# Optimization experiments

Measured on AMD Instinct MI355X. Metric: run time of the kernel, lower is better.

Reference implementation:

```python
import jax, jax.numpy as jnp
import numpy as np

B, T, D = 2, 2048, 1024
H, G, K = 16, 4, 64          # num_heads, num_kv_heads, head_dim
R = H // G                   # GQA repeat factor
F = 4096                     # mlp_dim
EPS = 1e-6


def rms_norm(x, scale, eps=EPS):
    var = jnp.mean(x.astype(jnp.float32) ** 2, axis=-1, keepdims=True)
    normed = x * jax.lax.rsqrt(var + eps)
    return (scale * normed).astype(x.dtype)


def apply_rope(x_BTHK, sin_BTK, cos_BTK):
    half = x_BTHK.shape[-1] // 2
    x1, x2 = x_BTHK[..., :half], x_BTHK[..., half:]
    s = sin_BTK[:, :, None, :]
    c = cos_BTK[:, :, None, :]
    return jnp.concatenate([x1 * c - x2 * s, x2 * c + x1 * s], axis=-1).astype(x_BTHK.dtype)


def setup_inputs() -> dict:
    key = jax.random.key(0)
    ks = jax.random.split(key, 12)
    hidden_BTD = jax.random.normal(ks[0], (B, T, D), jnp.float32)
    # rope tables: realistic sin/cos of position*inv_freq
    inv_freq = 1.0 / (10000.0 ** (jnp.arange(K // 2, dtype=jnp.float32) / (K // 2)))
    ang = jnp.arange(T, dtype=jnp.float32)[:, None] * inv_freq[None, :]  # [T, K/2]
    sin_BTK = jnp.broadcast_to(jnp.sin(ang)[None], (B, T, K // 2))
    cos_BTK = jnp.broadcast_to(jnp.cos(ang)[None], (B, T, K // 2))
    mask = jnp.broadcast_to(jnp.tril(jnp.ones((T, T), bool))[None], (B, T, T))
    sc = 1.0 / np.sqrt(D)
    scf = 1.0 / np.sqrt(F)
    return {
        "hidden_BTD": hidden_BTD, "sin_BTK": sin_BTK, "cos_BTK": cos_BTK, "mask": mask,
        "ln1_scale": jnp.ones((D,), jnp.float32),
        "ln2_scale": jnp.ones((D,), jnp.float32),
        "qn_scale": jnp.ones((K,), jnp.float32),
        "kn_scale": jnp.ones((K,), jnp.float32),
        "q_w": jax.random.normal(ks[1], (D, H * K), jnp.float32) * sc,
        "k_w": jax.random.normal(ks[2], (D, G * K), jnp.float32) * sc,
        "v_w": jax.random.normal(ks[3], (D, G * K), jnp.float32) * sc,
        "o_w": jax.random.normal(ks[4], (H * K, D), jnp.float32) * sc,
        "gate_w": jax.random.normal(ks[5], (D, F), jnp.float32) * sc,
        "up_w": jax.random.normal(ks[6], (D, F), jnp.float32) * sc,
        "down_w": jax.random.normal(ks[7], (F, D), jnp.float32) * scf,
    }


def reference(hidden_BTD, sin_BTK, cos_BTK, mask, ln1_scale, ln2_scale,
              qn_scale, kn_scale, q_w, k_w, v_w, o_w, gate_w, up_w, down_w):
    x = rms_norm(hidden_BTD, ln1_scale)
    q = rms_norm((x @ q_w).reshape(B, T, H, K), qn_scale)
    k = rms_norm((x @ k_w).reshape(B, T, G, K), kn_scale)
    v = (x @ v_w).reshape(B, T, G, K)
    q = apply_rope(q, sin_BTK, cos_BTK)
    k = apply_rope(k, sin_BTK, cos_BTK)
    q_BTGRK = q.reshape(B, T, G, R, K)
    scale = K ** (-0.5)
    logits = jnp.einsum('BTGRK,BSGK->BTSGR', q_BTGRK, k) * scale
    neg = float(jnp.finfo(logits.dtype).min)
    logits = jnp.where(mask[:, :, :, None, None], logits, neg)
    weights = jax.nn.softmax(logits.astype(jnp.float32), axis=2).astype(logits.dtype)
    attn = jnp.einsum('BTSGR,BSGK->BTGRK', weights, v).reshape(B, T, H * K)
    hidden_BTD = hidden_BTD + attn @ o_w
    y = rms_norm(hidden_BTD, ln2_scale)
    ff = (jax.nn.silu(y @ gate_w) * (y @ up_w)) @ down_w
    return hidden_BTD + ff
```

## Files before the change

kernel.cpp:

```cpp
#include <hip/hip_runtime.h>
#include <hip/hip_bf16.h>

#define EPSF 1e-6f
constexpr int Bsz  = 2;
constexpr int Tseq = 2048;
constexpr int Dmod = 1024;
constexpr int Hh   = 16;
constexpr int Gg   = 4;
constexpr int Ff   = 4096;
constexpr int Mrows = Bsz * Tseq;
constexpr int QKVN = 1536;

typedef __attribute__((ext_vector_type(8))) short bf16x8;
typedef __attribute__((ext_vector_type(4))) float f32x4;
typedef unsigned short u16;

__device__ inline u16 f2bf(float x) {
    union { float f; unsigned u; } v; v.f = x;
    unsigned r = v.u + 0x7fff + ((v.u >> 16) & 1);
    return (u16)(r >> 16);
}
__device__ inline float bf2f(u16 h) {
    union { unsigned u; float f; } v; v.u = ((unsigned)h) << 16; return v.f;
}

__device__ __forceinline__ void async_copy16(const u16* g, u16* l) {
    __builtin_amdgcn_global_load_lds(
        (const __attribute__((address_space(1))) void*)g,
        (__attribute__((address_space(3))) void*)l, 16, 0, 0);
}


template <int LO>
__global__ __launch_bounds__(256) void wprep_kernel(
    const float* __restrict__ W, u16* __restrict__ Th, u16* __restrict__ Tl,
    int Kd, int N)
{
    __shared__ float tile[32][33];
    const int n0 = blockIdx.x * 32, k0 = blockIdx.y * 32;
    const int r = threadIdx.x >> 3, c4 = (threadIdx.x & 7) * 4;
    const float4 v = *reinterpret_cast<const float4*>(&W[(size_t)(k0 + r) * N + n0 + c4]);
    tile[r][c4 + 0] = v.x; tile[r][c4 + 1] = v.y;
    tile[r][c4 + 2] = v.z; tile[r][c4 + 3] = v.w;
    __syncthreads();
    const int nl = threadIdx.x >> 3, kq = (threadIdx.x & 7) * 4;
    float x0 = tile[kq + 0][nl], x1 = tile[kq + 1][nl];
    float x2 = tile[kq + 2][nl], x3 = tile[kq + 3][nl];
    ushort4 h;
    h.x = f2bf(x0); h.y = f2bf(x1); h.z = f2bf(x2); h.w = f2bf(x3);
    *reinterpret_cast<ushort4*>(&Th[(size_t)(n0 + nl) * Kd + k0 + kq]) = h;
    if (LO) {
        ushort4 l;
        l.x = f2bf(x0 - bf2f(h.x)); l.y = f2bf(x1 - bf2f(h.y));
        l.z = f2bf(x2 - bf2f(h.z)); l.w = f2bf(x3 - bf2f(h.w));
        *reinterpret_cast<ushort4*>(&Tl[(size_t)(n0 + nl) * Kd + k0 + kq]) = l;
    }
}

template <int LO>
__global__ __launch_bounds__(256) void rmsnorm_split_kernel(
    const float* __restrict__ x, const float* __restrict__ scale,
    u16* __restrict__ oh, u16* __restrict__ ol)
{
    const int row = blockIdx.x;
    const int tid = threadIdx.x;
    const float4 v = reinterpret_cast<const float4*>(x + (size_t)row * Dmod)[tid];
    float ss = v.x * v.x + v.y * v.y + v.z * v.z + v.w * v.w;
    #pragma unroll
    for (int off = 32; off; off >>= 1) ss += __shfl_xor(ss, off, 64);
    __shared__ float part[4];
    if ((tid & 63) == 0) part[tid >> 6] = ss;
    __syncthreads();
    const float tot = part[0] + part[1] + part[2] + part[3];
    const float rstd = rsqrtf(tot * (1.0f / Dmod) + EPSF);
    const float4 sc = reinterpret_cast<const float4*>(scale)[tid];
    float o0 = v.x * rstd * sc.x, o1 = v.y * rstd * sc.y;
    float o2 = v.z * rstd * sc.z, o3 = v.w * rstd * sc.w;
    ushort4 h;
    h.x = f2bf(o0); h.y = f2bf(o1); h.z = f2bf(o2); h.w = f2bf(o3);
    *reinterpret_cast<ushort4*>(&oh[(size_t)row * Dmod + tid * 4]) = h;
    if (LO) {
        ushort4 l;
        l.x = f2bf(o0 - bf2f(h.x)); l.y = f2bf(o1 - bf2f(h.y));
        l.z = f2bf(o2 - bf2f(h.z)); l.w = f2bf(o3 - bf2f(h.w));
        *reinterpret_cast<ushort4*>(&ol[(size_t)row * Dmod + tid * 4]) = l;
    }
}

template <int ASPLIT, int BSPLIT, int RES>
__global__ __launch_bounds__(256, 2) void mfma_gemm_kernel(
    const u16* __restrict__ Ah, const u16* __restrict__ Al,
    const u16* __restrict__ Bh, const u16* __restrict__ Bl,
    const float* __restrict__ res, float* __restrict__ C,
    int M, int N, int Kd)
{
    __shared__ u16 As_h[128 * 32];
    __shared__ u16 As_l[128 * 32];
    __shared__ u16 Bs_h[128 * 32];
    __shared__ u16 Bs_l[128 * 32];

    const int tid = threadIdx.x;
    const int lane = tid & 63, wave = tid >> 6;
    const int wm = (wave >> 1) * 64, wn = (wave & 1) * 64;
    const int m0 = blockIdx.y * 128, n0 = blockIdx.x * 128;
    const int fm = lane & 15, quad = lane >> 4;
    const int fsw = (fm >> 1) & 3;
    const int fcol = ((quad ^ fsw) * 8);

    f32x4 acc[4][4];
    #pragma unroll
    for (int i = 0; i < 4; ++i)
        #pragma unroll
        for (int j = 0; j < 4; ++j) acc[i][j] = (f32x4){0.f, 0.f, 0.f, 0.f};

    const int lrow = lane >> 2;
    const int lchunk = lane & 3;
    const int schunk = lchunk ^ ((lrow >> 1) & 3);

    for (int k0 = 0; k0 < Kd; k0 += 32) {
        __syncthreads();
        #pragma unroll
        for (int p = 0; p < 2; ++p) {
            const int row = wave * 32 + p * 16 + lrow;
            const size_t ga = (size_t)(m0 + row) * Kd + k0 + schunk * 8;
            const size_t gb = (size_t)(n0 + row) * Kd + k0 + schunk * 8;
            const int ls = row * 32 + lchunk * 8;
            async_copy16(&Ah[ga], &As_h[ls]);
            if (ASPLIT) async_copy16(&Al[ga], &As_l[ls]);
            async_copy16(&Bh[gb], &Bs_h[ls]);
            if (BSPLIT) async_copy16(&Bl[gb], &Bs_l[ls]);
        }
        __syncthreads();

        bf16x8 ah[4], al[4], bh[4], bl[4];
        #pragma unroll
        for (int t = 0; t < 4; ++t) {
            const int ra = (wm + t * 16 + fm) * 32 + fcol;
            const int rb = (wn + t * 16 + fm) * 32 + fcol;
            ah[t] = *reinterpret_cast<const bf16x8*>(&As_h[ra]);
            bh[t] = *reinterpret_cast<const bf16x8*>(&Bs_h[rb]);
            if (ASPLIT) al[t] = *reinterpret_cast<const bf16x8*>(&As_l[ra]);
            if (BSPLIT) bl[t] = *reinterpret_cast<const bf16x8*>(&Bs_l[rb]);
        }
        #pragma unroll
        for (int mt = 0; mt < 4; ++mt)
            #pragma unroll
            for (int nt = 0; nt < 4; ++nt) {
                acc[mt][nt] = __builtin_amdgcn_mfma_f32_16x16x32_bf16(
                    ah[mt], bh[nt], acc[mt][nt], 0, 0, 0);
                if (BSPLIT)
                    acc[mt][nt] = __builtin_amdgcn_mfma_f32_16x16x32_bf16(
                        ah[mt], bl[nt], acc[mt][nt], 0, 0, 0);
                if (ASPLIT)
                    acc[mt][nt] = __builtin_amdgcn_mfma_f32_16x16x32_bf16(
                        al[mt], bh[nt], acc[mt][nt], 0, 0, 0);
            }
    }

    const int cr = (lane >> 4) * 4, cn = lane & 15;
    #pragma unroll
    for (int mt = 0; mt < 4; ++mt)
        #pragma unroll
        for (int nt = 0; nt < 4; ++nt)
            #pragma unroll
            for (int r = 0; r < 4; ++r) {
                const int gm = m0 + wm + mt * 16 + cr + r;
                const int gn = n0 + wn + nt * 16 + cn;
                float v = acc[mt][nt][r];
                if (RES) v += res[(size_t)gm * N + gn];
                C[(size_t)gm * N + gn] = v;
            }
}

__global__ __launch_bounds__(256, 2) void mfma_gateup_kernel(
    const u16* __restrict__ Ah, const u16* __restrict__ Al,
    const u16* __restrict__ Bg, const u16* __restrict__ Bu,
    u16* __restrict__ FF, int M, int N, int Kd)
{
    __shared__ u16 As_h[128 * 32];
    __shared__ u16 As_l[128 * 32];
    __shared__ u16 Gs[64 * 32];
    __shared__ u16 Us[64 * 32];

    const int tid = threadIdx.x;
    const int lane = tid & 63, wave = tid >> 6;
    const int wm = (wave >> 1) * 64, wn = (wave & 1) * 32;
    const int m0 = blockIdx.y * 128, n0 = blockIdx.x * 64;
    const int fm = lane & 15, quad = lane >> 4;
    const int fsw = (fm >> 1) & 3;
    const int fcol = ((quad ^ fsw) * 8);

    f32x4 accg[4][2], accu[4][2];
    #pragma unroll
    for (int i = 0; i < 4; ++i)
        #pragma unroll
        for (int j = 0; j < 2; ++j) {
            accg[i][j] = (f32x4){0.f, 0.f, 0.f, 0.f};
            accu[i][j] = (f32x4){0.f, 0.f, 0.f, 0.f};
        }

    const int lrow = lane >> 2;
    const int lchunk = lane & 3;
    const int schunk = lchunk ^ ((lrow >> 1) & 3);

    for (int k0 = 0; k0 < Kd; k0 += 32) {
        __syncthreads();
        #pragma unroll
        for (int p = 0; p < 2; ++p) {
            const int row = p * 64 + wave * 16 + lrow;
            const size_t ga = (size_t)(m0 + row) * Kd + k0 + schunk * 8;
            const int ls = row * 32 + lchunk * 8;
            async_copy16(&Ah[ga], &As_h[ls]);
            async_copy16(&Al[ga], &As_l[ls]);
        }
        {
            const int row = wave * 16 + lrow;
            const size_t gb = (size_t)(n0 + row) * Kd + k0 + schunk * 8;
            const int ls = row * 32 + lchunk * 8;
            async_copy16(&Bg[gb], &Gs[ls]);
            async_copy16(&Bu[gb], &Us[ls]);
        }
        __syncthreads();

        bf16x8 a_h[4], a_l[4], g_f[2], u_f[2];
        #pragma unroll
        for (int t = 0; t < 4; ++t) {
            const int ra = (wm + t * 16 + fm) * 32 + fcol;
            a_h[t] = *reinterpret_cast<const bf16x8*>(&As_h[ra]);
            a_l[t] = *reinterpret_cast<const bf16x8*>(&As_l[ra]);
        }
        #pragma unroll
        for (int j = 0; j < 2; ++j) {
            const int rb = (wn + j * 16 + fm) * 32 + fcol;
            g_f[j] = *reinterpret_cast<const bf16x8*>(&Gs[rb]);
            u_f[j] = *reinterpret_cast<const bf16x8*>(&Us[rb]);
        }
        #pragma unroll
        for (int mt = 0; mt < 4; ++mt)
            #pragma unroll
            for (int nt = 0; nt < 2; ++nt) {
                accg[mt][nt] = __builtin_amdgcn_mfma_f32_16x16x32_bf16(
                    a_h[mt], g_f[nt], accg[mt][nt], 0, 0, 0);
                accg[mt][nt] = __builtin_amdgcn_mfma_f32_16x16x32_bf16(
                    a_l[mt], g_f[nt], accg[mt][nt], 0, 0, 0);
                accu[mt][nt] = __builtin_amdgcn_mfma_f32_16x16x32_bf16(
                    a_h[mt], u_f[nt], accu[mt][nt], 0, 0, 0);
                accu[mt][nt] = __builtin_amdgcn_mfma_f32_16x16x32_bf16(
                    a_l[mt], u_f[nt], accu[mt][nt], 0, 0, 0);
            }
    }

    const int cr = (lane >> 4) * 4, cn = lane & 15;
    #pragma unroll
    for (int mt = 0; mt < 4; ++mt)
        #pragma unroll
        for (int nt = 0; nt < 2; ++nt)
            #pragma unroll
            for (int r = 0; r < 4; ++r) {
                const int gm = m0 + wm + mt * 16 + cr + r;
                const int gn = n0 + wn + nt * 16 + cn;
                const float g = accg[mt][nt][r];
                const float ff = (g / (1.0f + __expf(-g))) * accu[mt][nt][r];
                FF[(size_t)gm * N + gn] = f2bf(ff);
            }
}

__global__ __launch_bounds__(256) void qkrope_bf16_kernel(
    const float* __restrict__ src, const float* __restrict__ nsc,
    const float* __restrict__ sinp, const float* __restrict__ cosp,
    u16* __restrict__ outh, u16* __restrict__ outl,
    int NH, float oscale)
{
    const int lane = threadIdx.x & 63;
    const int w = threadIdx.x >> 6;
    const int head = blockIdx.x * 4 + w;
    const int bt = head / NH;
    const int h = head % NH;

    const float v = src[(size_t)bt * QKVN + h * 64 + lane];
    float ss = v * v;
    #pragma unroll
    for (int off = 32; off; off >>= 1) ss += __shfl_xor(ss, off, 64);
    const float rstd = rsqrtf(ss * (1.0f / 64.0f) + EPSF);
    const float nv = v * rstd * nsc[lane];

    const float p = __shfl_xor(nv, 32, 64);
    const float s = sinp[(size_t)bt * 32 + (lane & 31)];
    const float c = cosp[(size_t)bt * 32 + (lane & 31)];
    const float o = ((lane < 32) ? (nv * c - p * s) : (nv * c + p * s)) * oscale;

    const size_t oi = (size_t)bt * (NH * 64) + h * 64 + lane;
    const u16 hi = f2bf(o);
    outh[oi] = hi;
    outl[oi] = f2bf(o - bf2f(hi));
}

__global__ __launch_bounds__(256) void vtrans_kernel(
    const float* __restrict__ QKV, u16* __restrict__ Vth, u16* __restrict__ Vtl)
{
    __shared__ float tile[64][65];
    const int t0 = blockIdx.x * 64;
    const int bg = blockIdx.y;
    const int b = bg >> 2, g = bg & 3;
    const int tid = threadIdx.x;

    const int tl = tid >> 4, dq = (tid & 15) * 4;
    #pragma unroll
    for (int p = 0; p < 4; ++p) {
        const int t = tl + p * 16;
        const float4 v = *reinterpret_cast<const float4*>(
            &QKV[(size_t)(b * Tseq + t0 + t) * QKVN + 1280 + g * 64 + dq]);
        tile[t][dq + 0] = v.x; tile[t][dq + 1] = v.y;
        tile[t][dq + 2] = v.z; tile[t][dq + 3] = v.w;
    }
    __syncthreads();

    const int d = tid >> 2, tq = (tid & 3) * 16;
    u16 hv[16], lv[16];
    #pragma unroll
    for (int i = 0; i < 16; ++i) {
        const float v = tile[tq + i][d];
        hv[i] = f2bf(v);
        lv[i] = f2bf(v - bf2f(hv[i]));
    }
    const size_t oi = ((size_t)(bg * 64 + d)) * Tseq + t0 + tq;
    *reinterpret_cast<uint4*>(&Vth[oi])     = *reinterpret_cast<uint4*>(&hv[0]);
    *reinterpret_cast<uint4*>(&Vth[oi + 8]) = *reinterpret_cast<uint4*>(&hv[8]);
    *reinterpret_cast<uint4*>(&Vtl[oi])     = *reinterpret_cast<uint4*>(&lv[0]);
    *reinterpret_cast<uint4*>(&Vtl[oi + 8]) = *reinterpret_cast<uint4*>(&lv[8]);
}

__global__ __launch_bounds__(256) void attn_mfma_kernel(
    const u16* __restrict__ Qh, const u16* __restrict__ Ql,
    const u16* __restrict__ Kh, const u16* __restrict__ Kl,
    const u16* __restrict__ Vth, const u16* __restrict__ Vtl,
    u16* __restrict__ AOh, u16* __restrict__ AOl)
{
    __shared__ u16 KsH[64 * 72];
    __shared__ u16 KsL[64 * 72];
    __shared__ u16 VsH[64 * 72];
    __shared__ u16 VsL[64 * 72];
    __shared__ u16 Ps[4][16 * 72];

    const int tid = threadIdx.x;
    const int wave = tid >> 6, lane = tid & 63;
    const int l15 = lane & 15, quad = lane >> 4;

    const int bg = blockIdx.x & 7;
    const int b = bg >> 2, g = bg & 3;
    const int win = 127 - (blockIdx.x >> 3);
    const int t0 = win * 16;
    const int h = g * 4 + wave;

    bf16x8 qh[2], ql[2];
    {
        const size_t qrow = (size_t)(b * Tseq + t0 + l15) * 1024 + h * 64;
        #pragma unroll
        for (int ks = 0; ks < 2; ++ks) {
            qh[ks] = *reinterpret_cast<const bf16x8*>(&Qh[qrow + ks * 32 + quad * 8]);
            ql[ks] = *reinterpret_cast<const bf16x8*>(&Ql[qrow + ks * 32 + quad * 8]);
        }
    }

    const int srow = tid >> 2;
    const int scol = (tid & 3) * 16;
    const size_t kgb = (size_t)(b * Tseq) * 256 + g * 64 + scol;
    const size_t vgb = (size_t)(bg * 64 + srow) * Tseq + scol;

    const int nit = t0 / 64 + 1;

    uint4 ck0, ck1, cl0, cl1, cv0, cv1, cw0, cw1;
    {
        const size_t ka = kgb + (size_t)srow * 256;
        ck0 = *reinterpret_cast<const uint4*>(&Kh[ka]);
        ck1 = *reinterpret_cast<const uint4*>(&Kh[ka + 8]);
        cl0 = *reinterpret_cast<const uint4*>(&Kl[ka]);
        cl1 = *reinterpret_cast<const uint4*>(&Kl[ka + 8]);
        cv0 = *reinterpret_cast<const uint4*>(&Vth[vgb]);
        cv1 = *reinterpret_cast<const uint4*>(&Vth[vgb + 8]);
        cw0 = *reinterpret_cast<const uint4*>(&Vtl[vgb]);
        cw1 = *reinterpret_cast<const uint4*>(&Vtl[vgb + 8]);
    }

    f32x4 oacc[4];
    #pragma unroll
    for (int nt = 0; nt < 4; ++nt) oacc[nt] = (f32x4){0.f, 0.f, 0.f, 0.f};
    float m_r[4], l_r[4];
    #pragma unroll
    for (int r = 0; r < 4; ++r) { m_r[r] = -1e30f; l_r[r] = 0.0f; }

    u16* psw = &Ps[wave][0];
    const int lb = srow * 72 + scol;

    for (int it = 0; it < nit; ++it) {
        const int s0 = it * 64;
        const bool diag = (it == nit - 1);

        __syncthreads();
        *reinterpret_cast<uint4*>(&KsH[lb])     = ck0;
        *reinterpret_cast<uint4*>(&KsH[lb + 8]) = ck1;
        *reinterpret_cast<uint4*>(&KsL[lb])     = cl0;
        *reinterpret_cast<uint4*>(&KsL[lb + 8]) = cl1;
        *reinterpret_cast<uint4*>(&VsH[lb])     = cv0;
        *reinterpret_cast<uint4*>(&VsH[lb + 8]) = cv1;
        *reinterpret_cast<uint4*>(&VsL[lb])     = cw0;
        *reinterpret_cast<uint4*>(&VsL[lb + 8]) = cw1;
        if (it + 1 < nit) {
            const size_t ka = kgb + (size_t)(s0 + 64 + srow) * 256;
            ck0 = *reinterpret_cast<const uint4*>(&Kh[ka]);
            ck1 = *reinterpret_cast<const uint4*>(&Kh[ka + 8]);
            cl0 = *reinterpret_cast<const uint4*>(&Kl[ka]);
            cl1 = *reinterpret_cast<const uint4*>(&Kl[ka + 8]);
            const size_t va = vgb + s0 + 64;
            cv0 = *reinterpret_cast<const uint4*>(&Vth[va]);
            cv1 = *reinterpret_cast<const uint4*>(&Vth[va + 8]);
            cw0 = *reinterpret_cast<const uint4*>(&Vtl[va]);
            cw1 = *reinterpret_cast<const uint4*>(&Vtl[va + 8]);
        }
        __syncthreads();

        f32x4 sacc[4];
        #pragma unroll
        for (int nt = 0; nt < 4; ++nt) sacc[nt] = (f32x4){0.f, 0.f, 0.f, 0.f};

        #pragma unroll
        for (int ks = 0; ks < 2; ++ks) {
            bf16x8 kfh[4], kfl[4];
            #pragma unroll
            for (int nt = 0; nt < 4; ++nt) {
                const int a = (nt * 16 + l15) * 72 + ks * 32 + quad * 8;
                kfh[nt] = *reinterpret_cast<const bf16x8*>(&KsH[a]);
                kfl[nt] = *reinterpret_cast<const bf16x8*>(&KsL[a]);
            }
            #pragma unroll
            for (int nt = 0; nt < 4; ++nt) {
                sacc[nt] = __builtin_amdgcn_mfma_f32_16x16x32_bf16(qh[ks], kfh[nt], sacc[nt], 0, 0, 0);
                sacc[nt] = __builtin_amdgcn_mfma_f32_16x16x32_bf16(ql[ks], kfh[nt], sacc[nt], 0, 0, 0);
                sacc[nt] = __builtin_amdgcn_mfma_f32_16x16x32_bf16(qh[ks], kfl[nt], sacc[nt], 0, 0, 0);
            }
        }

        if (diag) {
            #pragma unroll
            for (int nt = 0; nt < 4; ++nt) {
                const int sg = s0 + nt * 16 + l15;
                #pragma unroll
                for (int r = 0; r < 4; ++r)
                    if (sg > t0 + quad * 4 + r) sacc[nt][r] = -1e30f;
            }
        }

        #pragma unroll
        for (int r = 0; r < 4; ++r) {
            float mx = fmaxf(fmaxf(sacc[0][r], sacc[1][r]),
                             fmaxf(sacc[2][r], sacc[3][r]));
            #pragma unroll
            for (int off = 1; off < 16; off <<= 1)
                mx = fmaxf(mx, __shfl_xor(mx, off, 16));
            const float mnew = fmaxf(m_r[r], mx);
            const float alpha = __expf(m_r[r] - mnew);
            m_r[r] = mnew;

            float rs = 0.0f;
            #pragma unroll
            for (int nt = 0; nt < 4; ++nt) {
                const float p = __expf(sacc[nt][r] - mnew);
                sacc[nt][r] = p;
                rs += p;
            }
            #pragma unroll
            for (int off = 1; off < 16; off <<= 1)
                rs += __shfl_xor(rs, off, 16);
            l_r[r] = l_r[r] * alpha + rs;
            #pragma unroll
            for (int nt = 0; nt < 4; ++nt) oacc[nt][r] *= alpha;
            #pragma unroll
            for (int nt = 0; nt < 4; ++nt)
                psw[(quad * 4 + r) * 72 + nt * 16 + l15] = f2bf(sacc[nt][r]);
        }

        #pragma unroll
        for (int ks = 0; ks < 2; ++ks) {
            const bf16x8 pa = *reinterpret_cast<const bf16x8*>(
                &psw[l15 * 72 + ks * 32 + quad * 8]);
            bf16x8 vfh[4], vfl[4];
            #pragma unroll
            for (int nt = 0; nt < 4; ++nt) {
                const int a = (nt * 16 + l15) * 72 + ks * 32 + quad * 8;
                vfh[nt] = *reinterpret_cast<const bf16x8*>(&VsH[a]);
                vfl[nt] = *reinterpret_cast<const bf16x8*>(&VsL[a]);
            }
            #pragma unroll
            for (int nt = 0; nt < 4; ++nt) {
                oacc[nt] = __builtin_amdgcn_mfma_f32_16x16x32_bf16(pa, vfh[nt], oacc[nt], 0, 0, 0);
                oacc[nt] = __builtin_amdgcn_mfma_f32_16x16x32_bf16(pa, vfl[nt], oacc[nt], 0, 0, 0);
            }
        }
    }

    #pragma unroll
    for (int r = 0; r < 4; ++r) {
        const float inv = 1.0f / l_r[r];
        const size_t orow = (size_t)(b * Tseq + t0 + quad * 4 + r) * 1024 + h * 64;
        #pragma unroll
        for (int nt = 0; nt < 4; ++nt) {
            const float o = oacc[nt][r] * inv;
            const u16 hi = f2bf(o);
            AOh[orow + nt * 16 + l15] = hi;
            AOl[orow + nt * 16 + l15] = f2bf(o - bf2f(hi));
        }
    }
}

extern "C" void kernel_launch(void* const* d_in, const int* in_sizes, int n_in,
                              void* d_out, int out_size, void* d_ws,
                              size_t ws_size, hipStream_t stream)
{
    const float* hidden = (const float*)d_in[0];
    const float* sinp   = (const float*)d_in[1];
    const float* cosp   = (const float*)d_in[2];
    const float* ln1    = (const float*)d_in[4];
    const float* ln2    = (const float*)d_in[5];
    const float* qn     = (const float*)d_in[6];
    const float* kn     = (const float*)d_in[7];
    const float* q_w    = (const float*)d_in[8];
    const float* k_w    = (const float*)d_in[9];
    const float* v_w    = (const float*)d_in[10];
    const float* o_w    = (const float*)d_in[11];
    const float* gate_w = (const float*)d_in[12];
    const float* up_w   = (const float*)d_in[13];
    const float* down_w = (const float*)d_in[14];
    float* out = (float*)d_out;

    char* base = (char*)d_ws;
    u16*   OTh  = (u16*)(base);
    u16*   OTl  = (u16*)(base + 2097152);
    u16*   GTh  = (u16*)(base + 4194304);
    u16*   UTh  = (u16*)(base + 12582912);
    u16*   DTh  = (u16*)(base + 20971520);
    float* QKV  = (float*)(base + 29360128);
    u16*   Qbh  = (u16*)(base + 54525952);
    u16*   Qbl  = (u16*)(base + 62914560);
    u16*   FFh  = (u16*)(base + 71303168);
    u16*   QKVT = (u16*)(base + 104857600);
    u16*   Xh   = (u16*)(base + 108003328);

    u16*   Kbh  = QKVT;
    u16*   Kbl  = Kbh + (size_t)4096 * 256;
    u16*   Vth  = Kbl + (size_t)4096 * 256;
    u16*   Vtl  = Vth + (size_t)8 * 64 * 2048;
    u16*   AOh  = (u16*)QKV;
    u16*   AOl  = AOh + (size_t)4096 * 1024;
    u16*   Yl   = (u16*)(base + 29360128 + 16777216);
    float* H2   = (float*)Qbh;
    u16*   Yh   = Kbh;

    wprep_kernel<0><<<dim3(32, 32), 256, 0, stream>>>(q_w, QKVT, nullptr, 1024, 1024);
    wprep_kernel<0><<<dim3(8, 32), 256, 0, stream>>>(k_w, QKVT + (size_t)1024 * 1024, nullptr, 1024, 256);
    wprep_kernel<0><<<dim3(8, 32), 256, 0, stream>>>(v_w, QKVT + (size_t)1280 * 1024, nullptr, 1024, 256);
    wprep_kernel<1><<<dim3(32, 32), 256, 0, stream>>>(o_w, OTh, OTl, 1024, 1024);
    wprep_kernel<0><<<dim3(128, 32), 256, 0, stream>>>(gate_w, GTh, nullptr, 1024, 4096);
    wprep_kernel<0><<<dim3(128, 32), 256, 0, stream>>>(up_w, UTh, nullptr, 1024, 4096);
    wprep_kernel<0><<<dim3(32, 128), 256, 0, stream>>>(down_w, DTh, nullptr, 4096, 1024);

    rmsnorm_split_kernel<0><<<Mrows, 256, 0, stream>>>(hidden, ln1, Xh, nullptr);

    mfma_gemm_kernel<0, 0, 0><<<dim3(QKVN / 128, Mrows / 128), 256, 0, stream>>>(
        Xh, nullptr, QKVT, nullptr, nullptr, QKV, Mrows, QKVN, 1024);

    qkrope_bf16_kernel<<<Mrows * Hh / 4, 256, 0, stream>>>(
        QKV, qn, sinp, cosp, Qbh, Qbl, Hh, 0.125f);
    qkrope_bf16_kernel<<<Mrows * Gg / 4, 256, 0, stream>>>(
        QKV + 1024, kn, sinp, cosp, Kbh, Kbl, Gg, 1.0f);
    vtrans_kernel<<<dim3(Tseq / 64, Bsz * Gg), 256, 0, stream>>>(QKV, Vth, Vtl);

    attn_mfma_kernel<<<Bsz * Gg * (Tseq / 16), 256, 0, stream>>>(
        Qbh, Qbl, Kbh, Kbl, Vth, Vtl, AOh, AOl);

    mfma_gemm_kernel<1, 1, 1><<<dim3(8, 32), 256, 0, stream>>>(
        AOh, AOl, OTh, OTl, hidden, H2, Mrows, Dmod, 1024);

    rmsnorm_split_kernel<1><<<Mrows, 256, 0, stream>>>(H2, ln2, Yh, Yl);

    mfma_gateup_kernel<<<dim3(Ff / 64, Mrows / 128), 256, 0, stream>>>(
        Yh, Yl, GTh, UTh, FFh, Mrows, Ff, 1024);

    mfma_gemm_kernel<0, 0, 1><<<dim3(8, 32), 256, 0, stream>>>(
        FFh, nullptr, DTh, nullptr, H2, out, Mrows, Dmod, 4096);
}
```

Measured before the change: 561.7 us.

## Fuse QK norm and RoPE into QKV GEMM epilogue and merge weight prep launches

The QKV projection GEMM now applies per-head RMS norm, RoPE and the hi/lo bf16 split directly in its epilogue, so the fp32 QKV intermediate is never written and read back. V is emitted as bf16 hi/lo and transposed by a new bf16 transpose kernel. Weight prep for q/k/v and for gate/up is merged into single launches. This cuts memory traffic and launch count, at the cost of scattered 2-byte epilogue stores and a heavier GEMM epilogue.

```diff
diff --git a/kernel.cpp b/kernel.cpp
--- a/kernel.cpp
+++ b/kernel.cpp
@@ -9,7 +9,6 @@
 constexpr int Gg   = 4;
 constexpr int Ff   = 4096;
 constexpr int Mrows = Bsz * Tseq;
-constexpr int QKVN = 1536;
 
 typedef __attribute__((ext_vector_type(8))) short bf16x8;
 typedef __attribute__((ext_vector_type(4))) float f32x4;
@@ -57,6 +56,49 @@
     }
 }
 
+__global__ __launch_bounds__(256) void wprep_qkv_kernel(
+    const float* __restrict__ q_w, const float* __restrict__ k_w,
+    const float* __restrict__ v_w, u16* __restrict__ QKVT)
+{
+    const int nx = blockIdx.x;
+    const float* W; int N, n0s, drow;
+    if (nx < 32)      { W = q_w; N = 1024; n0s = nx * 32;        drow = nx * 32; }
+    else if (nx < 40) { W = k_w; N = 256;  n0s = (nx - 32) * 32; drow = 1024 + (nx - 32) * 32; }
+    else              { W = v_w; N = 256;  n0s = (nx - 40) * 32; drow = 1280 + (nx - 40) * 32; }
+    const int k0 = blockIdx.y * 32;
+    __shared__ float tile[32][33];
+    const int r = threadIdx.x >> 3, c4 = (threadIdx.x & 7) * 4;
+    const float4 v = *reinterpret_cast<const float4*>(&W[(size_t)(k0 + r) * N + n0s + c4]);
+    tile[r][c4 + 0] = v.x; tile[r][c4 + 1] = v.y;
+    tile[r][c4 + 2] = v.z; tile[r][c4 + 3] = v.w;
+    __syncthreads();
+    const int nl = threadIdx.x >> 3, kq = (threadIdx.x & 7) * 4;
+    ushort4 h;
+    h.x = f2bf(tile[kq + 0][nl]); h.y = f2bf(tile[kq + 1][nl]);
+    h.z = f2bf(tile[kq + 2][nl]); h.w = f2bf(tile[kq + 3][nl]);
+    *reinterpret_cast<ushort4*>(&QKVT[(size_t)(drow + nl) * 1024 + k0 + kq]) = h;
+}
+
+__global__ __launch_bounds__(256) void wprep_gu_kernel(
+    const float* __restrict__ gate_w, const float* __restrict__ up_w,
+    u16* __restrict__ GTh, u16* __restrict__ UTh)
+{
+    const float* W = blockIdx.z ? up_w : gate_w;
+    u16* T = blockIdx.z ? UTh : GTh;
+    const int n0 = blockIdx.x * 32, k0 = blockIdx.y * 32;
+    __shared__ float tile[32][33];
+    const int r = threadIdx.x >> 3, c4 = (threadIdx.x & 7) * 4;
+    const float4 v = *reinterpret_cast<const float4*>(&W[(size_t)(k0 + r) * 4096 + n0 + c4]);
+    tile[r][c4 + 0] = v.x; tile[r][c4 + 1] = v.y;
+    tile[r][c4 + 2] = v.z; tile[r][c4 + 3] = v.w;
+    __syncthreads();
+    const int nl = threadIdx.x >> 3, kq = (threadIdx.x & 7) * 4;
+    ushort4 h;
+    h.x = f2bf(tile[kq + 0][nl]); h.y = f2bf(tile[kq + 1][nl]);
+    h.z = f2bf(tile[kq + 2][nl]); h.w = f2bf(tile[kq + 3][nl]);
+    *reinterpret_cast<ushort4*>(&T[(size_t)(n0 + nl) * 1024 + k0 + kq]) = h;
+}
+
 template <int LO>
 __global__ __launch_bounds__(256) void rmsnorm_split_kernel(
     const float* __restrict__ x, const float* __restrict__ scale,
@@ -172,6 +214,169 @@
             }
 }
 
+__global__ __launch_bounds__(256, 2) void qkv_fused_kernel(
+    const u16* __restrict__ Ah, const u16* __restrict__ Bh,
+    const float* __restrict__ qn, const float* __restrict__ kn,
+    const float* __restrict__ sinp, const float* __restrict__ cosp,
+    u16* __restrict__ Qbh, u16* __restrict__ Qbl,
+    u16* __restrict__ Kbh, u16* __restrict__ Kbl,
+    u16* __restrict__ Vbh, u16* __restrict__ Vbl)
+{
+    __shared__ u16 As_h[128 * 32];
+    __shared__ u16 Bs_h[128 * 32];
+
+    const int Kd = 1024;
+    const int tid = threadIdx.x;
+    const int lane = tid & 63, wave = tid >> 6;
+    const int wm = (wave >> 1) * 64, wn = (wave & 1) * 64;
+    const int m0 = blockIdx.y * 128, n0 = blockIdx.x * 128;
+    const int fm = lane & 15, quad = lane >> 4;
+    const int fsw = (fm >> 1) & 3;
+    const int fcol = ((quad ^ fsw) * 8);
+
+    f32x4 acc[4][4];
+    #pragma unroll
+    for (int i = 0; i < 4; ++i)
+        #pragma unroll
+        for (int j = 0; j < 4; ++j) acc[i][j] = (f32x4){0.f, 0.f, 0.f, 0.f};
+
+    const int lrow = lane >> 2;
+    const int lchunk = lane & 3;
+    const int schunk = lchunk ^ ((lrow >> 1) & 3);
+
+    for (int k0 = 0; k0 < Kd; k0 += 32) {
+        __syncthreads();
+        #pragma unroll
+        for (int p = 0; p < 2; ++p) {
+            const int row = wave * 32 + p * 16 + lrow;
+            const size_t ga = (size_t)(m0 + row) * Kd + k0 + schunk * 8;
+            const size_t gb = (size_t)(n0 + row) * Kd + k0 + schunk * 8;
+            const int ls = row * 32 + lchunk * 8;
+            async_copy16(&Ah[ga], &As_h[ls]);
+            async_copy16(&Bh[gb], &Bs_h[ls]);
+        }
+        __syncthreads();
+
+        bf16x8 ah[4], bh[4];
+        #pragma unroll
+        for (int t = 0; t < 4; ++t) {
+            ah[t] = *reinterpret_cast<const bf16x8*>(&As_h[(wm + t * 16 + fm) * 32 + fcol]);
+            bh[t] = *reinterpret_cast<const bf16x8*>(&Bs_h[(wn + t * 16 + fm) * 32 + fcol]);
+        }
+        #pragma unroll
+        for (int mt = 0; mt < 4; ++mt)
+            #pragma unroll
+            for (int nt = 0; nt < 4; ++nt)
+                acc[mt][nt] = __builtin_amdgcn_mfma_f32_16x16x32_bf16(
+                    ah[mt], bh[nt], acc[mt][nt], 0, 0, 0);
+    }
+
+    const int gn0 = n0 + wn;
+    const int l15 = lane & 15;
+
+    if (gn0 < 1280) {
+        const bool isQ = (gn0 < 1024);
+        const float* nsc = isQ ? qn : kn;
+        const float osc = isQ ? 0.125f : 1.0f;
+        u16* __restrict__ oh = isQ ? Qbh : Kbh;
+        u16* __restrict__ ol = isQ ? Qbl : Kbl;
+        const int rowstride = isQ ? 1024 : 256;
+        const int colbase = isQ ? gn0 : gn0 - 1024;
+        float sc[4];
+        #pragma unroll
+        for (int nt = 0; nt < 4; ++nt) sc[nt] = nsc[nt * 16 + l15];
+
+        #pragma unroll
+        for (int mt = 0; mt < 4; ++mt)
+            #pragma unroll
+            for (int r = 0; r < 4; ++r) {
+                const int bt = m0 + wm + mt * 16 + quad * 4 + r;
+                float v[4];
+                #pragma unroll
+                for (int nt = 0; nt < 4; ++nt) v[nt] = acc[mt][nt][r];
+                float ss = v[0] * v[0] + v[1] * v[1] + v[2] * v[2] + v[3] * v[3];
+                #pragma unroll
+                for (int off = 1; off < 16; off <<= 1)
+                    ss += __shfl_xor(ss, off, 16);
+                const float rstd = rsqrtf(ss * (1.0f / 64.0f) + EPSF);
+                float nv[4];
+                #pragma unroll
+                for (int nt = 0; nt < 4; ++nt) nv[nt] = v[nt] * rstd * sc[nt];
+                const float s0 = sinp[bt * 32 + l15];
+                const float c0 = cosp[bt * 32 + l15];
+                const float s1 = sinp[bt * 32 + 16 + l15];
+                const float c1 = cosp[bt * 32 + 16 + l15];
+                float o[4];
+                o[0] = (nv[0] * c0 - nv[2] * s0) * osc;
+                o[1] = (nv[1] * c1 - nv[3] * s1) * osc;
+                o[2] = (nv[2] * c0 + nv[0] * s0) * osc;
+                o[3] = (nv[3] * c1 + nv[1] * s1) * osc;
+                #pragma unroll
+                for (int nt = 0; nt < 4; ++nt) {
+                    const size_t off = (size_t)bt * rowstride + colbase + nt * 16 + l15;
+                    const u16 hi = f2bf(o[nt]);
+                    oh[off] = hi;
+                    ol[off] = f2bf(o[nt] - bf2f(hi));
+                }
+            }
+    } else {
+        const int colbase = gn0 - 1280;
+        #pragma unroll
+        for (int mt = 0; mt < 4; ++mt)
+            #pragma unroll
+            for (int r = 0; r < 4; ++r) {
+                const int bt = m0 + wm + mt * 16 + quad * 4 + r;
+                #pragma unroll
+                for (int nt = 0; nt < 4; ++nt) {
+                    const float v = acc[mt][nt][r];
+                    const size_t off = (size_t)bt * 256 + colbase + nt * 16 + l15;
+                    const u16 hi = f2bf(v);
+                    Vbh[off] = hi;
+                    Vbl[off] = f2bf(v - bf2f(hi));
+                }
+            }
+    }
+}
+
+__global__ __launch_bounds__(256) void vtrans_bf16_kernel(
+    const u16* __restrict__ Vbh, const u16* __restrict__ Vbl,
+    u16* __restrict__ Vth, u16* __restrict__ Vtl)
+{
+    __shared__ u16 th[64 * 66];
+    __shared__ u16 tl[64 * 66];
+    const int t0 = blockIdx.x * 64;
+    const int bg = blockIdx.y;
+    const int b = bg >> 2, g = bg & 3;
+    const int tid = threadIdx.x;
+
+    const int row = tid >> 2;
+    const int cc = (tid & 3) * 16;
+    const size_t src = (size_t)(b * Tseq + t0 + row) * 256 + g * 64 + cc;
+    *reinterpret_cast<uint4*>(&th[row * 66 + cc]) =
+        *reinterpret_cast<const uint4*>(&Vbh[src]);
+    *reinterpret_cast<uint4*>(&th[row * 66 + cc + 8]) =
+        *reinterpret_cast<const uint4*>(&Vbh[src + 8]);
+    *reinterpret_cast<uint4*>(&tl[row * 66 + cc]) =
+        *reinterpret_cast<const uint4*>(&Vbl[src]);
+    *reinterpret_cast<uint4*>(&tl[row * 66 + cc + 8]) =
+        *reinterpret_cast<const uint4*>(&Vbl[src + 8]);
+    __syncthreads();
+
+    const int d = tid >> 2;
+    const int tq = (tid & 3) * 16;
+    u16 oh[16], ol[16];
+    #pragma unroll
+    for (int i = 0; i < 16; ++i) {
+        oh[i] = th[(tq + i) * 66 + d];
+        ol[i] = tl[(tq + i) * 66 + d];
+    }
+    const size_t dst = (size_t)(bg * 64 + d) * Tseq + t0 + tq;
+    *reinterpret_cast<uint4*>(&Vth[dst])     = *reinterpret_cast<uint4*>(&oh[0]);
+    *reinterpret_cast<uint4*>(&Vth[dst + 8]) = *reinterpret_cast<uint4*>(&oh[8]);
+    *reinterpret_cast<uint4*>(&Vtl[dst])     = *reinterpret_cast<uint4*>(&ol[0]);
+    *reinterpret_cast<uint4*>(&Vtl[dst + 8]) = *reinterpret_cast<uint4*>(&ol[8]);
+}
+
 __global__ __launch_bounds__(256, 2) void mfma_gateup_kernel(
     const u16* __restrict__ Ah, const u16* __restrict__ Al,
     const u16* __restrict__ Bg, const u16* __restrict__ Bu,
@@ -263,71 +468,6 @@
                 const float ff = (g / (1.0f + __expf(-g))) * accu[mt][nt][r];
                 FF[(size_t)gm * N + gn] = f2bf(ff);
             }
-}
-
-__global__ __launch_bounds__(256) void qkrope_bf16_kernel(
-    const float* __restrict__ src, const float* __restrict__ nsc,
-    const float* __restrict__ sinp, const float* __restrict__ cosp,
-    u16* __restrict__ outh, u16* __restrict__ outl,
-    int NH, float oscale)
-{
-    const int lane = threadIdx.x & 63;
-    const int w = threadIdx.x >> 6;
-    const int head = blockIdx.x * 4 + w;
-    const int bt = head / NH;
-    const int h = head % NH;
-
-    const float v = src[(size_t)bt * QKVN + h * 64 + lane];
-    float ss = v * v;
-    #pragma unroll
-    for (int off = 32; off; off >>= 1) ss += __shfl_xor(ss, off, 64);
-    const float rstd = rsqrtf(ss * (1.0f / 64.0f) + EPSF);
-    const float nv = v * rstd * nsc[lane];
-
-    const float p = __shfl_xor(nv, 32, 64);
-    const float s = sinp[(size_t)bt * 32 + (lane & 31)];
-    const float c = cosp[(size_t)bt * 32 + (lane & 31)];
-    const float o = ((lane < 32) ? (nv * c - p * s) : (nv * c + p * s)) * oscale;
-
-    const size_t oi = (size_t)bt * (NH * 64) + h * 64 + lane;
-    const u16 hi = f2bf(o);
-    outh[oi] = hi;
-    outl[oi] = f2bf(o - bf2f(hi));
-}
-
-__global__ __launch_bounds__(256) void vtrans_kernel(
-    const float* __restrict__ QKV, u16* __restrict__ Vth, u16* __restrict__ Vtl)
-{
-    __shared__ float tile[64][65];
-    const int t0 = blockIdx.x * 64;
-    const int bg = blockIdx.y;
-    const int b = bg >> 2, g = bg & 3;
-    const int tid = threadIdx.x;
-
-    const int tl = tid >> 4, dq = (tid & 15) * 4;
-    #pragma unroll
-    for (int p = 0; p < 4; ++p) {
-        const int t = tl + p * 16;
-        const float4 v = *reinterpret_cast<const float4*>(
-            &QKV[(size_t)(b * Tseq + t0 + t) * QKVN + 1280 + g * 64 + dq]);
-        tile[t][dq + 0] = v.x; tile[t][dq + 1] = v.y;
-        tile[t][dq + 2] = v.z; tile[t][dq + 3] = v.w;
-    }
-    __syncthreads();
-
-    const int d = tid >> 2, tq = (tid & 3) * 16;
-    u16 hv[16], lv[16];
-    #pragma unroll
-    for (int i = 0; i < 16; ++i) {
-        const float v = tile[tq + i][d];
-        hv[i] = f2bf(v);
-        lv[i] = f2bf(v - bf2f(hv[i]));
-    }
-    const size_t oi = ((size_t)(bg * 64 + d)) * Tseq + t0 + tq;
-    *reinterpret_cast<uint4*>(&Vth[oi])     = *reinterpret_cast<uint4*>(&hv[0]);
-    *reinterpret_cast<uint4*>(&Vth[oi + 8]) = *reinterpret_cast<uint4*>(&hv[8]);
-    *reinterpret_cast<uint4*>(&Vtl[oi])     = *reinterpret_cast<uint4*>(&lv[0]);
-    *reinterpret_cast<uint4*>(&Vtl[oi + 8]) = *reinterpret_cast<uint4*>(&lv[8]);
 }
 
 __global__ __launch_bounds__(256) void attn_mfma_kernel(
@@ -538,41 +678,36 @@
     u16*   GTh  = (u16*)(base + 4194304);
     u16*   UTh  = (u16*)(base + 12582912);
     u16*   DTh  = (u16*)(base + 20971520);
-    float* QKV  = (float*)(base + 29360128);
-    u16*   Qbh  = (u16*)(base + 54525952);
-    u16*   Qbl  = (u16*)(base + 62914560);
-    u16*   FFh  = (u16*)(base + 71303168);
-    u16*   QKVT = (u16*)(base + 104857600);
-    u16*   Xh   = (u16*)(base + 108003328);
-
-    u16*   Kbh  = QKVT;
-    u16*   Kbl  = Kbh + (size_t)4096 * 256;
-    u16*   Vth  = Kbl + (size_t)4096 * 256;
-    u16*   Vtl  = Vth + (size_t)8 * 64 * 2048;
-    u16*   AOh  = (u16*)QKV;
-    u16*   AOl  = AOh + (size_t)4096 * 1024;
-    u16*   Yl   = (u16*)(base + 29360128 + 16777216);
-    float* H2   = (float*)Qbh;
-    u16*   Yh   = Kbh;
-
-    wprep_kernel<0><<<dim3(32, 32), 256, 0, stream>>>(q_w, QKVT, nullptr, 1024, 1024);
-    wprep_kernel<0><<<dim3(8, 32), 256, 0, stream>>>(k_w, QKVT + (size_t)1024 * 1024, nullptr, 1024, 256);
-    wprep_kernel<0><<<dim3(8, 32), 256, 0, stream>>>(v_w, QKVT + (size_t)1280 * 1024, nullptr, 1024, 256);
+    u16*   QKVT = (u16*)(base + 29360128);
+    u16*   Xh   = (u16*)(base + 32505856);
+    u16*   Qbh  = (u16*)(base + 40894464);
+    u16*   Qbl  = (u16*)(base + 49283072);
+    u16*   Kbh  = (u16*)(base + 57671680);
+    u16*   Kbl  = (u16*)(base + 59768832);
+    u16*   Vbh  = (u16*)(base + 61865984);
+    u16*   Vbl  = (u16*)(base + 63963136);
+    u16*   Vth  = (u16*)(base + 66060288);
+    u16*   Vtl  = (u16*)(base + 68157440);
+    u16*   AOh  = (u16*)(base + 70254592);
+    u16*   AOl  = (u16*)(base + 78643200);
+    u16*   FFh  = (u16*)(base + 87031808);
+
+    float* H2 = (float*)Qbh;
+    u16*   Yh = Kbh;
+    u16*   Yl = Vth;
+
+    wprep_qkv_kernel<<<dim3(48, 32), 256, 0, stream>>>(q_w, k_w, v_w, QKVT);
     wprep_kernel<1><<<dim3(32, 32), 256, 0, stream>>>(o_w, OTh, OTl, 1024, 1024);
-    wprep_kernel<0><<<dim3(128, 32), 256, 0, stream>>>(gate_w, GTh, nullptr, 1024, 4096);
-    wprep_kernel<0><<<dim3(128, 32), 256, 0, stream>>>(up_w, UTh, nullptr, 1024, 4096);
+    wprep_gu_kernel<<<dim3(128, 32, 2), 256, 0, stream>>>(gate_w, up_w, GTh, UTh);
     wprep_kernel<0><<<dim3(32, 128), 256, 0, stream>>>(down_w, DTh, nullptr, 4096, 1024);
 
     rmsnorm_split_kernel<0><<<Mrows, 256, 0, stream>>>(hidden, ln1, Xh, nullptr);
 
-    mfma_gemm_kernel<0, 0, 0><<<dim3(QKVN / 128, Mrows / 128), 256, 0, stream>>>(
-        Xh, nullptr, QKVT, nullptr, nullptr, QKV, Mrows, QKVN, 1024);
-
-    qkrope_bf16_kernel<<<Mrows * Hh / 4, 256, 0, stream>>>(
-        QKV, qn, sinp, cosp, Qbh, Qbl, Hh, 0.125f);
-    qkrope_bf16_kernel<<<Mrows * Gg / 4, 256, 0, stream>>>(
-        QKV + 1024, kn, sinp, cosp, Kbh, Kbl, Gg, 1.0f);
-    vtrans_kernel<<<dim3(Tseq / 64, Bsz * Gg), 256, 0, stream>>>(QKV, Vth, Vtl);
+    qkv_fused_kernel<<<dim3(12, 32), 256, 0, stream>>>(
+        Xh, QKVT, qn, kn, sinp, cosp, Qbh, Qbl, Kbh, Kbl, Vbh, Vbl);
+
+    vtrans_bf16_kernel<<<dim3(Tseq / 64, Bsz * Gg), 256, 0, stream>>>(
+        Vbh, Vbl, Vth, Vtl);
 
     attn_mfma_kernel<<<Bsz * Gg * (Tseq / 16), 256, 0, stream>>>(
         Qbh, Qbl, Kbh, Kbl, Vth, Vtl, AOh, AOl);
```

New measurement: 543.8 us. -3.2%, faster.
